# Kernel optimization log

Hardware: AMD Instinct MI355X
Metric: run time of the kernel (lower is better)

The kernel has to match this reference:

```python
import jax, jax.numpy as jnp
import numpy as np

FOLD_SIZE = 16
FOLDS = 4
LEVELS = 4
LEN_KEEP_LEVEL = 128
SCALE = 8
BASE = jnp.asarray((SCALE ** np.arange(4)[::-1]).astype(np.float32))  # [512,64,8,1]


def setup_inputs() -> dict:
    key = jax.random.key(0)
    x = jax.random.normal(key, (16, 3, 1024, 1024), dtype=jnp.float32)
    return {"x": x}


def _patchify(x):
    B, C, H, W = x.shape
    H -= H % FOLD_SIZE
    W -= W % FOLD_SIZE
    x = x[:, :, :H, :W]
    ph, pw = H // FOLD_SIZE, W // FOLD_SIZE
    p = x.reshape(B, C, ph, FOLD_SIZE, pw, FOLD_SIZE)
    p = p.transpose(0, 2, 4, 1, 3, 5).reshape(B, ph * pw, C, FOLD_SIZE, FOLD_SIZE)
    return p, ph, pw


def _diag_diff(p):
    # |triu(p) - rot90(flip(tril(p), axis=1), -1)| summed over patch dims
    a = jnp.triu(p)
    b = jnp.rot90(jnp.flip(jnp.tril(p), axis=1), -1, axes=(1, 2))
    return jnp.abs(a - b).sum((1, 2))


def _get_direction(patches):
    # patches: [N, fs, fs]
    fs = FOLD_SIZE
    half = fs // 2
    sq_tri = (fs * fs - fs) / 2.0
    sq = fs * fs / 2.0
    d0 = _diag_diff(patches) / sq_tri
    d1 = _diag_diff(jnp.rot90(patches, -1, axes=(1, 2))) / sq_tri
    d2 = jnp.abs(patches[:, :, :half] - patches[:, :, half:]).sum((1, 2)) / sq
    d3 = jnp.abs(patches[:, :half, :] - patches[:, half:, :]).sum((1, 2)) / sq
    directions = jnp.stack([d0, d1, d2, d3], axis=-1)  # [N,4]
    direction = jnp.argmin(directions, axis=-1)
    one_hot = jax.nn.one_hot(direction, 4, dtype=jnp.int32)
    return direction.astype(jnp.int32), one_hot


def _fold(direction, one_hot):
    # 8-neighbor stencil: pad with sentinel 4 (never a valid direction)
    pd = jnp.pad(direction, ((0, 0), (1, 1), (1, 1)), constant_values=4)
    s7, s8, s9 = pd[:, :-2, :-2], pd[:, :-2, 1:-1], pd[:, :-2, 2:]
    s4, s6 = pd[:, 1:-1, :-2], pd[:, 1:-1, 2:]
    s1, s2, s3 = pd[:, 2:, :-2], pd[:, 2:, 1:-1], pd[:, 2:, 2:]
    scope = one_hot.sum(-1)  # computed BEFORE updates, as in the original
    valid = (direction != 4).astype(jnp.int32)
    eq = lambda s: (direction == s).astype(jnp.int32)
    add = jnp.stack([eq(s9) + eq(s1), eq(s7) + eq(s3), eq(s8) + eq(s2), eq(s4) + eq(s6)], axis=-1)
    return one_hot + (scope * valid)[..., None] * add


def reference(x):
    patches, Hp, Wp = _patchify(x)
    B = patches.shape[0]
    p = patches.mean(2).reshape(B * Hp * Wp, FOLD_SIZE, FOLD_SIZE)
    direction, one_hot = _get_direction(p)
    direction = direction.reshape(B, Hp, Wp)
    one_hot = one_hot.reshape(B, Hp, Wp, 4)
    for _ in range(FOLDS):
        one_hot = _fold(direction, one_hot)
    scope = one_hot.sum(-1).reshape(B, Hp * Wp)
    one_hot = one_hot.reshape(B, Hp * Wp, 4)
    # center = flattened argmax of scope; original uses //H and %H (H==W here)
    idx = jnp.argmax(scope, axis=-1)
    center = jnp.stack([idx // Hp, idx % Hp], axis=1)[:, None, :]  # [B,1,2]
    hh, ww = jnp.meshgrid(jnp.arange(Hp), jnp.arange(Wp), indexing='ij')
    cord = jnp.stack([hh, ww], axis=-1).reshape(-1, 2)  # [HW,2]
    distance = ((center - cord[None]) ** 2).sum(-1)  # [B,HW]
    index = jnp.argsort(-distance, axis=-1)  # descending
    oh = jnp.take_along_axis(one_hot, index[..., None], axis=1).astype(jnp.float32)
    token = oh / oh.sum(-1, keepdims=True)
    token = jnp.minimum(jnp.round(token * SCALE), float(SCALE))
    L = token.shape[1]
    token = token[:, : L - L % LEVELS].reshape(B, LEVELS, -1, 4)
    token = (BASE * token).sum(-1).astype(jnp.int32)  # [B,levels,L/levels]
    token = jnp.concatenate([token[:, i, :LEN_KEEP_LEVEL] for i in range(LEVELS)], axis=1)
    return token  # [B, levels*len_keep_level] int tokens
```

## Files before the change

kernel.cpp:

```cpp
#include <hip/hip_runtime.h>
#include <hip/hip_bf16.h>


__global__ __launch_bounds__(256) void k_dir(const float* __restrict__ x,
                                             int* __restrict__ dir) {
    int t = threadIdx.x;
    int wave = t >> 6, lane = t & 63;
    int P = blockIdx.x * 4 + wave;
    int b = P >> 12, pid = P & 4095;
    int ph = pid >> 6, pw = pid & 63;
    int i = lane >> 2, j0 = (lane & 3) << 2;

    const float* base = x + (size_t)b * 3145728 + (size_t)(ph * 16 + i) * 1024 + pw * 16 + j0;
    float4 a0 = *(const float4*)(base);
    float4 a1 = *(const float4*)(base + 1048576);
    float4 a2 = *(const float4*)(base + 2097152);

    __shared__ float pl[4][16][17];
    float* row = &pl[wave][i][j0];
    row[0] = (a0.x + a1.x + a2.x) / 3.0f;
    row[1] = (a0.y + a1.y + a2.y) / 3.0f;
    row[2] = (a0.z + a1.z + a2.z) / 3.0f;
    row[3] = (a0.w + a1.w + a2.w) / 3.0f;
    __syncthreads();

    const float (*p)[17] = pl[wave];
    double c0 = 0.0, c1 = 0.0, c2 = 0.0, c3 = 0.0;
#pragma unroll
    for (int q = 0; q < 4; ++q) {
        int j = j0 + q;
        float pij = p[i][j];
        if (j > i) {
            c0 += (double)fabsf(pij - p[j][i]);
            c1 += (double)fabsf(p[15 - j][i] - p[15 - i][j]);
        }
        if (j < 8) c2 += (double)fabsf(pij - p[i][j + 8]);
        if (i < 8) c3 += (double)fabsf(pij - p[i + 8][j]);
    }
#pragma unroll
    for (int off = 32; off > 0; off >>= 1) {
        c0 += __shfl_xor(c0, off, 64);
        c1 += __shfl_xor(c1, off, 64);
        c2 += __shfl_xor(c2, off, 64);
        c3 += __shfl_xor(c3, off, 64);
    }
    if (lane == 0) {
        double d0 = c0 / 120.0;
        double d1 = c1 / 120.0;
        double d2 = c2 / 128.0;
        double d3 = c3 / 128.0;
        int dm = 0; double best = d0;
        if (d1 < best) { best = d1; dm = 1; }
        if (d2 < best) { best = d2; dm = 2; }
        if (d3 < best) { best = d3; dm = 3; }
        dir[P] = dm;
    }
}

__global__ __launch_bounds__(256) void k_fold(const int* __restrict__ dir,
                                              int* __restrict__ oh,
                                              int* __restrict__ scope) {
    int P = blockIdx.x * 256 + threadIdx.x;
    int b = P >> 12, pid = P & 4095;
    int h = pid >> 6, w = pid & 63;
    const int* db = dir + b * 4096;
    int d = db[pid];

    auto get = [&](int hh, int ww) -> int {
        if (hh < 0 || hh > 63 || ww < 0 || ww > 63) return 4;
        return db[hh * 64 + ww];
    };
    int e_ul = (get(h - 1, w - 1) == d), e_u  = (get(h - 1, w) == d), e_ur = (get(h - 1, w + 1) == d);
    int e_l  = (get(h,     w - 1) == d),                              e_r  = (get(h,     w + 1) == d);
    int e_dl = (get(h + 1, w - 1) == d), e_dn = (get(h + 1, w) == d), e_dr = (get(h + 1, w + 1) == d);

    int add0 = e_ur + e_dl;
    int add1 = e_ul + e_dr;
    int add2 = e_u  + e_dn;
    int add3 = e_l  + e_r;
    int A = add0 + add1 + add2 + add3;
    int s = 1 + A;
    int s2 = s * s;
    int S = 1 + s + s2 + s2 * s;

    oh[P * 4 + 0] = (d == 0) + add0 * S;
    oh[P * 4 + 1] = (d == 1) + add1 * S;
    oh[P * 4 + 2] = (d == 2) + add2 * S;
    oh[P * 4 + 3] = (d == 3) + add3 * S;
    scope[P] = s2 * s2;
}

__global__ __launch_bounds__(256) void k_center(const int* __restrict__ scope,
                                                int* __restrict__ center) {
    int b = blockIdx.x;
    int t = threadIdx.x;
    const int* sb = scope + b * 4096;
    int bv = -1, bi = 0;
    for (int k = t; k < 4096; k += 256) {
        int v = sb[k];
        if (v > bv) { bv = v; bi = k; }
    }
#pragma unroll
    for (int off = 32; off > 0; off >>= 1) {
        int ov = __shfl_xor(bv, off, 64);
        int oi = __shfl_xor(bi, off, 64);
        if (ov > bv || (ov == bv && oi < bi)) { bv = ov; bi = oi; }
    }
    __shared__ int sv[4], si[4];
    int wave = t >> 6, lane = t & 63;
    if (lane == 0) { sv[wave] = bv; si[wave] = bi; }
    __syncthreads();
    if (t == 0) {
        for (int wv = 1; wv < 4; ++wv)
            if (sv[wv] > bv || (sv[wv] == bv && si[wv] < bi)) { bv = sv[wv]; bi = si[wv]; }
        center[b] = bi;
    }
}

__global__ __launch_bounds__(256) void k_token(const int* __restrict__ oh,
                                               const int* __restrict__ center,
                                               int* __restrict__ out) {
    int b = blockIdx.x >> 4;
    int slice = blockIdx.x & 15;
    int t = threadIdx.x;
    int idx = center[b];
    int ch = idx >> 6, cw = idx & 63;

    __shared__ int keys[4096];
#pragma unroll
    for (int q = 0; q < 16; ++q) {
        int j = q * 256 + t;
        int h = j >> 6, w = j & 63;
        int dh = ch - h, dw = cw - w;
        int d = dh * dh + dw * dw;
        keys[j] = ((8191 - d) << 12) | j;
    }
    __syncthreads();

    int k = slice * 256 + t;
    int h = k >> 6, w = k & 63;
    int dh = ch - h, dw = cw - w;
    int d = dh * dh + dw * dw;
    int mykey = ((8191 - d) << 12) | k;

    int rank = 0;
    const int4* k4 = (const int4*)keys;
    for (int j = 0; j < 1024; ++j) {
        int4 v = k4[j];
        rank += (v.x < mykey) + (v.y < mykey) + (v.z < mykey) + (v.w < mykey);
    }

    int level = rank >> 10, pil = rank & 1023;
    if (pil < 128) {
        int P = b * 4096 + k;
        int o0 = oh[P * 4 + 0], o1 = oh[P * 4 + 1], o2 = oh[P * 4 + 2], o3 = oh[P * 4 + 3];
        float sum = (float)(o0 + o1 + o2 + o3);
        float t0 = fminf(rintf(((float)o0 / sum) * 8.0f), 8.0f);
        float t1 = fminf(rintf(((float)o1 / sum) * 8.0f), 8.0f);
        float t2 = fminf(rintf(((float)o2 / sum) * 8.0f), 8.0f);
        float t3 = fminf(rintf(((float)o3 / sum) * 8.0f), 8.0f);
        float tok = 512.0f * t0 + 64.0f * t1 + 8.0f * t2 + t3;
        out[b * 512 + (level << 7) + pil] = (int)tok;
    }
}

extern "C" void kernel_launch(void* const* d_in, const int* in_sizes, int n_in,
                              void* d_out, int out_size, void* d_ws, size_t ws_size,
                              hipStream_t stream) {
    const float* x = (const float*)d_in[0];
    int* out = (int*)d_out;

    char* ws = (char*)d_ws;
    int* dir    = (int*)(ws);
    int* oh     = (int*)(ws + (256 << 10));
    int* scope  = (int*)(ws + (256 << 10) + (1 << 20));
    int* center = (int*)(ws + (256 << 10) + (1 << 20) + (256 << 10));

    k_dir   <<<16384, 256, 0, stream>>>(x, dir);
    k_fold  <<<256,   256, 0, stream>>>(dir, oh, scope);
    k_center<<<16,    256, 0, stream>>>(scope, center);
    k_token <<<256,   256, 0, stream>>>(oh, center, out);
}
```

Baseline: 312.3 us.

## Fuse center argmax into fold kernel via packed-key atomicMax

Removes the separate center-finding kernel. The fold kernel packs scope and inverted index into one int key, reduces it per block with shuffles, and combines blocks with atomicMax. k_dir initializes the key buffer. The token kernel also uses vectorized int4 loads/stores for the one-hot data and splits the rank counter into four accumulators with unrolling. This saves one launch and some memory traffic, at the cost of depending on k_dir having reset the keys and on the scope value fitting in the upper bits of the key.

```diff
diff --git a/kernel.cpp b/kernel.cpp
--- a/kernel.cpp
+++ b/kernel.cpp
@@ -3,8 +3,10 @@
 
 
 __global__ __launch_bounds__(256) void k_dir(const float* __restrict__ x,
-                                             int* __restrict__ dir) {
+                                             int* __restrict__ dir,
+                                             int* __restrict__ centerkey) {
     int t = threadIdx.x;
+    if (blockIdx.x == 0 && t < 16) centerkey[t] = -1;
     int wave = t >> 6, lane = t & 63;
     int P = blockIdx.x * 4 + wave;
     int b = P >> 12, pid = P & 4095;
@@ -57,9 +59,9 @@
     }
 }
 
-__global__ __launch_bounds__(256) void k_fold(const int* __restrict__ dir,
-                                              int* __restrict__ oh,
-                                              int* __restrict__ scope) {
+__global__ __launch_bounds__(256) void k_foldcenter(const int* __restrict__ dir,
+                                                    int* __restrict__ oh,
+                                                    int* __restrict__ centerkey) {
     int P = blockIdx.x * 256 + threadIdx.x;
     int b = P >> 12, pid = P & 4095;
     int h = pid >> 6, w = pid & 63;
@@ -70,95 +72,70 @@
         if (hh < 0 || hh > 63 || ww < 0 || ww > 63) return 4;
         return db[hh * 64 + ww];
     };
-    int e_ul = (get(h - 1, w - 1) == d), e_u  = (get(h - 1, w) == d), e_ur = (get(h - 1, w + 1) == d);
-    int e_l  = (get(h,     w - 1) == d),                              e_r  = (get(h,     w + 1) == d);
-    int e_dl = (get(h + 1, w - 1) == d), e_dn = (get(h + 1, w) == d), e_dr = (get(h + 1, w + 1) == d);
-
-    int add0 = e_ur + e_dl;
-    int add1 = e_ul + e_dr;
-    int add2 = e_u  + e_dn;
-    int add3 = e_l  + e_r;
-    int A = add0 + add1 + add2 + add3;
-    int s = 1 + A;
+    int add0 = (get(h - 1, w + 1) == d) + (get(h + 1, w - 1) == d);
+    int add1 = (get(h - 1, w - 1) == d) + (get(h + 1, w + 1) == d);
+    int add2 = (get(h - 1, w) == d) + (get(h + 1, w) == d);
+    int add3 = (get(h, w - 1) == d) + (get(h, w + 1) == d);
+    int s = 1 + add0 + add1 + add2 + add3;
     int s2 = s * s;
     int S = 1 + s + s2 + s2 * s;
 
-    oh[P * 4 + 0] = (d == 0) + add0 * S;
-    oh[P * 4 + 1] = (d == 1) + add1 * S;
-    oh[P * 4 + 2] = (d == 2) + add2 * S;
-    oh[P * 4 + 3] = (d == 3) + add3 * S;
-    scope[P] = s2 * s2;
-}
+    ((int4*)oh)[P] = make_int4((d == 0) + add0 * S, (d == 1) + add1 * S,
+                               (d == 2) + add2 * S, (d == 3) + add3 * S);
 
-__global__ __launch_bounds__(256) void k_center(const int* __restrict__ scope,
-                                                int* __restrict__ center) {
-    int b = blockIdx.x;
-    int t = threadIdx.x;
-    const int* sb = scope + b * 4096;
-    int bv = -1, bi = 0;
-    for (int k = t; k < 4096; k += 256) {
-        int v = sb[k];
-        if (v > bv) { bv = v; bi = k; }
-    }
+    int key = (s2 * s2 << 12) | (4095 - pid);
 #pragma unroll
-    for (int off = 32; off > 0; off >>= 1) {
-        int ov = __shfl_xor(bv, off, 64);
-        int oi = __shfl_xor(bi, off, 64);
-        if (ov > bv || (ov == bv && oi < bi)) { bv = ov; bi = oi; }
-    }
-    __shared__ int sv[4], si[4];
-    int wave = t >> 6, lane = t & 63;
-    if (lane == 0) { sv[wave] = bv; si[wave] = bi; }
+    for (int off = 32; off > 0; off >>= 1)
+        key = max(key, __shfl_xor(key, off, 64));
+    __shared__ int wmax[4];
+    if ((threadIdx.x & 63) == 0) wmax[threadIdx.x >> 6] = key;
     __syncthreads();
-    if (t == 0) {
-        for (int wv = 1; wv < 4; ++wv)
-            if (sv[wv] > bv || (sv[wv] == bv && si[wv] < bi)) { bv = sv[wv]; bi = si[wv]; }
-        center[b] = bi;
-    }
+    if (threadIdx.x == 0)
+        atomicMax(&centerkey[b], max(max(wmax[0], wmax[1]), max(wmax[2], wmax[3])));
 }
 
 __global__ __launch_bounds__(256) void k_token(const int* __restrict__ oh,
-                                               const int* __restrict__ center,
+                                               const int* __restrict__ centerkey,
                                                int* __restrict__ out) {
     int b = blockIdx.x >> 4;
     int slice = blockIdx.x & 15;
     int t = threadIdx.x;
-    int idx = center[b];
+    int idx = 4095 - (centerkey[b] & 4095);
     int ch = idx >> 6, cw = idx & 63;
 
     __shared__ int keys[4096];
 #pragma unroll
     for (int q = 0; q < 16; ++q) {
         int j = q * 256 + t;
-        int h = j >> 6, w = j & 63;
-        int dh = ch - h, dw = cw - w;
-        int d = dh * dh + dw * dw;
-        keys[j] = ((8191 - d) << 12) | j;
+        int dh = ch - (j >> 6), dw = cw - (j & 63);
+        keys[j] = ((8191 - (dh * dh + dw * dw)) << 12) | j;
     }
     __syncthreads();
 
     int k = slice * 256 + t;
-    int h = k >> 6, w = k & 63;
-    int dh = ch - h, dw = cw - w;
-    int d = dh * dh + dw * dw;
-    int mykey = ((8191 - d) << 12) | k;
+    int dh = ch - (k >> 6), dw = cw - (k & 63);
+    int mykey = ((8191 - (dh * dh + dw * dw)) << 12) | k;
 
-    int rank = 0;
+    int r0 = 0, r1 = 0, r2 = 0, r3 = 0;
     const int4* k4 = (const int4*)keys;
+#pragma unroll 8
     for (int j = 0; j < 1024; ++j) {
         int4 v = k4[j];
-        rank += (v.x < mykey) + (v.y < mykey) + (v.z < mykey) + (v.w < mykey);
+        r0 += (v.x < mykey);
+        r1 += (v.y < mykey);
+        r2 += (v.z < mykey);
+        r3 += (v.w < mykey);
     }
+    int rank = (r0 + r1) + (r2 + r3);
 
     int level = rank >> 10, pil = rank & 1023;
     if (pil < 128) {
-        int P = b * 4096 + k;
-        int o0 = oh[P * 4 + 0], o1 = oh[P * 4 + 1], o2 = oh[P * 4 + 2], o3 = oh[P * 4 + 3];
-        float sum = (float)(o0 + o1 + o2 + o3);
-        float t0 = fminf(rintf(((float)o0 / sum) * 8.0f), 8.0f);
-        float t1 = fminf(rintf(((float)o1 / sum) * 8.0f), 8.0f);
-        float t2 = fminf(rintf(((float)o2 / sum) * 8.0f), 8.0f);
-        float t3 = fminf(rintf(((float)o3 / sum) * 8.0f), 8.0f);
+        int4 o = ((const int4*)oh)[b * 4096 + k];
+        float sum = (float)(o.x + o.y + o.z + o.w);
+        float t0 = fminf(rintf(((float)o.x / sum) * 8.0f), 8.0f);
+        float t1 = fminf(rintf(((float)o.y / sum) * 8.0f), 8.0f);
+        float t2 = fminf(rintf(((float)o.z / sum) * 8.0f), 8.0f);
+        float t3 = fminf(rintf(((float)o.w / sum) * 8.0f), 8.0f);
         float tok = 512.0f * t0 + 64.0f * t1 + 8.0f * t2 + t3;
         out[b * 512 + (level << 7) + pil] = (int)tok;
     }
@@ -171,13 +148,11 @@
     int* out = (int*)d_out;
 
     char* ws = (char*)d_ws;
-    int* dir    = (int*)(ws);
-    int* oh     = (int*)(ws + (256 << 10));
-    int* scope  = (int*)(ws + (256 << 10) + (1 << 20));
-    int* center = (int*)(ws + (256 << 10) + (1 << 20) + (256 << 10));
+    int* dir       = (int*)(ws);
+    int* oh        = (int*)(ws + (256 << 10));
+    int* centerkey = (int*)(ws + (256 << 10) + (1 << 20));
 
-    k_dir   <<<16384, 256, 0, stream>>>(x, dir);
-    k_fold  <<<256,   256, 0, stream>>>(dir, oh, scope);
-    k_center<<<16,    256, 0, stream>>>(scope, center);
-    k_token <<<256,   256, 0, stream>>>(oh, center, out);
+    k_dir       <<<16384, 256, 0, stream>>>(x, dir, centerkey);
+    k_foldcenter<<<256,   256, 0, stream>>>(dir, oh, centerkey);
+    k_token     <<<256,   256, 0, stream>>>(oh, centerkey, out);
 }
```

Result: faster. 301.0 us (-3.6%).
